# Kernel optimization log

Measured on AMD Instinct MI355X. Metric: run time of the kernel, lower is better.

## Reference

```python
import jax, jax.numpy as jnp
import numpy as np

K = 7       # kernel_size (window is K x K, padding=(K-1)//2, stride=1)
HEADS = 4   # number of heads; mid_channels = C // HEADS


def _unfold(x, k):
    # Emulates nn.Unfold(k, padding=(k-1)//2, stride=1) followed by reshape to
    # (B, C, P, H, W) with P = k*k ordered as (ki, kj) per channel (torch order).
    B, C, H, W = x.shape
    p = (k - 1) // 2
    xp = jnp.pad(x, ((0, 0), (0, 0), (p, p), (p, p)))  # zeros padding_mode
    patches = [xp[:, :, i:i + H, j:j + W] for i in range(k) for j in range(k)]
    return jnp.stack(patches, axis=2)  # (B, C, P, H, W)


def setup_inputs() -> dict:
    key = jax.random.key(0)
    x = jax.random.normal(key, (4, 64, 128, 128), dtype=jnp.float32)
    return {"x": x}


def reference(x):
    B, C, H, W = x.shape
    mid = C // HEADS
    P = K * K
    # (B, heads, mid, P, H, W)
    x_unf = _unfold(x, K).reshape(B, HEADS, mid, P, H, W)
    x_r = x.reshape(B, HEADS, mid, H, W)
    # squared L2 distance between center pixel feature and each window patch pixel
    A = ((x_unf ** 2).sum(axis=2)
         + (x_r ** 2).sum(axis=2, keepdims=True)
         - 2.0 * jnp.einsum('bgcphw,bgchw->bgphw', x_unf, x_r))  # (B,G,P,H,W)
    A = jax.nn.softmax(-A, axis=2)
    y = jnp.einsum('bgphw,bgcphw->bgchw', A, x_unf).reshape(B, C, H, W)
    return x + y  # residual=True
```

## Files before the change

### kernel.cpp

```cpp
#include <hip/hip_runtime.h>


#define TILE 16
#define RAD  3
#define HALO (TILE + 2 * RAD)
#define MID  16
#define NPIX (HALO * HALO)
#define IMG  128
#define HW   (IMG * IMG)
#define PSTR 20

__global__ __launch_bounds__(256, 4)
void nlm_kernel(const float* __restrict__ x, float* __restrict__ out) {
    const int g   = blockIdx.z & 3;
    const int b   = blockIdx.z >> 2;
    const int tx0 = blockIdx.x * TILE;
    const int ty0 = blockIdx.y * TILE;

    __shared__ __align__(16) float lds[NPIX * PSTR];

    const int tid = threadIdx.x;
    const float* xb = x + (size_t)(b * 64 + g * MID) * HW;

    for (int i = tid; i < NPIX * MID; i += 256) {
        const int c   = i / NPIX;
        const int pix = i - c * NPIX;
        const int yy  = pix / HALO;
        const int xx  = pix - yy * HALO;
        const int gy  = ty0 + yy - RAD;
        const int gx  = tx0 + xx - RAD;
        float v = 0.0f;
        if ((unsigned)gy < (unsigned)IMG && (unsigned)gx < (unsigned)IMG)
            v = xb[c * HW + gy * IMG + gx];
        lds[pix * PSTR + c] = v;
    }
    __syncthreads();

    for (int pix = tid; pix < NPIX; pix += 256) {
        const float* p = &lds[pix * PSTR];
        float ss = 0.0f;
        #pragma unroll
        for (int k = 0; k < 4; ++k) {
            const float4 v = *reinterpret_cast<const float4*>(p + 4 * k);
            ss = fmaf(v.x, v.x, ss); ss = fmaf(v.y, v.y, ss);
            ss = fmaf(v.z, v.z, ss); ss = fmaf(v.w, v.w, ss);
        }
        lds[pix * PSTR + MID] = ss;
    }
    __syncthreads();

    const int lx = tid & 15;
    const int ly = tid >> 4;
    const float* base = &lds[(ly * HALO + lx) * PSTR];

    float ctr[MID];
    {
        const float* cp = base + (RAD * HALO + RAD) * PSTR;
        #pragma unroll
        for (int k = 0; k < 4; ++k) {
            const float4 v = *reinterpret_cast<const float4*>(cp + 4 * k);
            ctr[4 * k + 0] = v.x; ctr[4 * k + 1] = v.y;
            ctr[4 * k + 2] = v.z; ctr[4 * k + 3] = v.w;
        }
    }
    const float cc = base[(RAD * HALO + RAD) * PSTR + MID];

    float acc[MID];
    #pragma unroll
    for (int c = 0; c < MID; ++c) acc[c] = 0.0f;
    float s = 0.0f;

    #pragma unroll
    for (int dy = 0; dy < 7; ++dy) {
        #pragma unroll
        for (int dx = 0; dx < 7; ++dx) {
            const float* nbp = base + (dy * HALO + dx) * PSTR;
            float nb[MID];
            #pragma unroll
            for (int k = 0; k < 4; ++k) {
                const float4 v = *reinterpret_cast<const float4*>(nbp + 4 * k);
                nb[4 * k + 0] = v.x; nb[4 * k + 1] = v.y;
                nb[4 * k + 2] = v.z; nb[4 * k + 3] = v.w;
            }
            const float nn = nbp[MID];
            float dot = 0.0f;
            #pragma unroll
            for (int c = 0; c < MID; ++c) dot = fmaf(nb[c], ctr[c], dot);
            const float w = __expf(fmaf(2.0f, dot, -(nn + cc)));
            s += w;
            #pragma unroll
            for (int c = 0; c < MID; ++c) acc[c] = fmaf(w, nb[c], acc[c]);
        }
    }

    const float inv = 1.0f / s;
    float* ob = out + (size_t)(b * 64 + g * MID) * HW
                    + (size_t)(ty0 + ly) * IMG + (tx0 + lx);
    #pragma unroll
    for (int c = 0; c < MID; ++c)
        ob[c * HW] = fmaf(acc[c], inv, ctr[c]);
}

extern "C" void kernel_launch(void* const* d_in, const int* in_sizes, int n_in,
                              void* d_out, int out_size, void* d_ws, size_t ws_size,
                              hipStream_t stream) {
    const float* x = (const float*)d_in[0];
    float* out = (float*)d_out;
    dim3 grid(IMG / TILE, IMG / TILE, 16);
    nlm_kernel<<<grid, 256, 0, stream>>>(x, out);
}
```

Before: 34.67 us.

## Compute two vertically adjacent pixels per thread to share neighbor LDS loads

Each thread now computes two vertically stacked output pixels, so each neighbor row loaded from LDS serves both pixels across the 8 overlapping window rows. The tile grows to 16x32 with a 22x38 halo, the halo fill loads 4 channels per thread and writes them as a float4, and squared norms move to a separate LDS array. This cuts LDS reads per pixel, at the cost of doubled accumulator registers, lower occupancy (launch bounds 2), half as many blocks, and more LDS per block.

New measurement: 29.58 us. 14.7% less time.

```diff
diff --git a/kernel.cpp b/kernel.cpp
--- a/kernel.cpp
+++ b/kernel.cpp
@@ -1,104 +1,145 @@
 #include <hip/hip_runtime.h>
 
 
-#define TILE 16
+#define TW   16
+#define TH   32
 #define RAD  3
-#define HALO (TILE + 2 * RAD)
+#define HWD  22
+#define HHT  38
 #define MID  16
-#define NPIX (HALO * HALO)
+#define NPIX (HWD * HHT)
+#define PSTR 20
 #define IMG  128
-#define HW   (IMG * IMG)
-#define PSTR 20
+#define PLANE (IMG * IMG)
 
-__global__ __launch_bounds__(256, 4)
+#define VISIT(RP, NP, WX, DO0, DO1)                                         \
+    {                                                                       \
+        const float* _rp = (RP) + (WX) * PSTR;                              \
+        float nb[MID];                                                      \
+        _Pragma("unroll")                                                   \
+        for (int k = 0; k < 4; ++k) {                                       \
+            const float4 v = *reinterpret_cast<const float4*>(_rp + 4 * k); \
+            nb[4*k+0] = v.x; nb[4*k+1] = v.y;                               \
+            nb[4*k+2] = v.z; nb[4*k+3] = v.w;                               \
+        }                                                                   \
+        const float nv = (NP)[WX];                                          \
+        if (DO0) {                                                          \
+            float dot = 0.f;                                                \
+            _Pragma("unroll")                                               \
+            for (int c = 0; c < MID; ++c) dot = fmaf(nb[c], ctr0[c], dot);  \
+            const float w = __expf(fmaf(2.f, dot, -(nv + cc0)));            \
+            s0 += w;                                                        \
+            _Pragma("unroll")                                               \
+            for (int c = 0; c < MID; ++c) acc0[c] = fmaf(w, nb[c], acc0[c]);\
+        }                                                                   \
+        if (DO1) {                                                          \
+            float dot = 0.f;                                                \
+            _Pragma("unroll")                                               \
+            for (int c = 0; c < MID; ++c) dot = fmaf(nb[c], ctr1[c], dot);  \
+            const float w = __expf(fmaf(2.f, dot, -(nv + cc1)));            \
+            s1 += w;                                                        \
+            _Pragma("unroll")                                               \
+            for (int c = 0; c < MID; ++c) acc1[c] = fmaf(w, nb[c], acc1[c]);\
+        }                                                                   \
+    }
+
+__global__ __launch_bounds__(256, 2)
 void nlm_kernel(const float* __restrict__ x, float* __restrict__ out) {
     const int g   = blockIdx.z & 3;
     const int b   = blockIdx.z >> 2;
-    const int tx0 = blockIdx.x * TILE;
-    const int ty0 = blockIdx.y * TILE;
+    const int tx0 = blockIdx.x * TW;
+    const int ty0 = blockIdx.y * TH;
 
-    __shared__ __align__(16) float lds[NPIX * PSTR];
+    __shared__ __align__(16) float rec[NPIX * PSTR];
+    __shared__ float nn[NPIX];
 
     const int tid = threadIdx.x;
-    const float* xb = x + (size_t)(b * 64 + g * MID) * HW;
+    const float* xb = x + (size_t)(b * 64 + g * MID) * PLANE;
 
-    for (int i = tid; i < NPIX * MID; i += 256) {
-        const int c   = i / NPIX;
-        const int pix = i - c * NPIX;
-        const int yy  = pix / HALO;
-        const int xx  = pix - yy * HALO;
+    for (int i = tid; i < 4 * NPIX; i += 256) {
+        const int cq  = i / NPIX;
+        const int pix = i - cq * NPIX;
+        const int yy  = pix / HWD;
+        const int xx  = pix - yy * HWD;
         const int gy  = ty0 + yy - RAD;
         const int gx  = tx0 + xx - RAD;
-        float v = 0.0f;
-        if ((unsigned)gy < (unsigned)IMG && (unsigned)gx < (unsigned)IMG)
-            v = xb[c * HW + gy * IMG + gx];
-        lds[pix * PSTR + c] = v;
+        float4 v = make_float4(0.f, 0.f, 0.f, 0.f);
+        if ((unsigned)gy < (unsigned)IMG && (unsigned)gx < (unsigned)IMG) {
+            const float* p = xb + (size_t)(4 * cq) * PLANE + gy * IMG + gx;
+            v.x = p[0];         v.y = p[PLANE];
+            v.z = p[2 * PLANE]; v.w = p[3 * PLANE];
+        }
+        *reinterpret_cast<float4*>(&rec[pix * PSTR + 4 * cq]) = v;
     }
     __syncthreads();
 
     for (int pix = tid; pix < NPIX; pix += 256) {
-        const float* p = &lds[pix * PSTR];
-        float ss = 0.0f;
+        const float* p = &rec[pix * PSTR];
+        float ss = 0.f;
         #pragma unroll
         for (int k = 0; k < 4; ++k) {
             const float4 v = *reinterpret_cast<const float4*>(p + 4 * k);
             ss = fmaf(v.x, v.x, ss); ss = fmaf(v.y, v.y, ss);
             ss = fmaf(v.z, v.z, ss); ss = fmaf(v.w, v.w, ss);
         }
-        lds[pix * PSTR + MID] = ss;
+        nn[pix] = ss;
     }
     __syncthreads();
 
-    const int lx = tid & 15;
-    const int ly = tid >> 4;
-    const float* base = &lds[(ly * HALO + lx) * PSTR];
+    const int lx  = tid & 15;
+    const int ly  = tid >> 4;
+    const int p00 = (2 * ly) * HWD + lx;
 
-    float ctr[MID];
+    float ctr0[MID], ctr1[MID];
     {
-        const float* cp = base + (RAD * HALO + RAD) * PSTR;
+        const float* c0 = &rec[(p00 + 3 * HWD + 3) * PSTR];
         #pragma unroll
         for (int k = 0; k < 4; ++k) {
-            const float4 v = *reinterpret_cast<const float4*>(cp + 4 * k);
-            ctr[4 * k + 0] = v.x; ctr[4 * k + 1] = v.y;
-            ctr[4 * k + 2] = v.z; ctr[4 * k + 3] = v.w;
+            const float4 v0 = *reinterpret_cast<const float4*>(c0 + 4 * k);
+            const float4 v1 = *reinterpret_cast<const float4*>(c0 + HWD * PSTR + 4 * k);
+            ctr0[4*k+0] = v0.x; ctr0[4*k+1] = v0.y;
+            ctr0[4*k+2] = v0.z; ctr0[4*k+3] = v0.w;
+            ctr1[4*k+0] = v1.x; ctr1[4*k+1] = v1.y;
+            ctr1[4*k+2] = v1.z; ctr1[4*k+3] = v1.w;
         }
     }
-    const float cc = base[(RAD * HALO + RAD) * PSTR + MID];
+    const float cc0 = nn[p00 + 3 * HWD + 3];
+    const float cc1 = nn[p00 + 4 * HWD + 3];
 
-    float acc[MID];
+    float acc0[MID], acc1[MID];
     #pragma unroll
-    for (int c = 0; c < MID; ++c) acc[c] = 0.0f;
-    float s = 0.0f;
+    for (int c = 0; c < MID; ++c) { acc0[c] = 0.f; acc1[c] = 0.f; }
+    float s0 = 0.f, s1 = 0.f;
 
-    #pragma unroll
-    for (int dy = 0; dy < 7; ++dy) {
+    {
+        const float* rp = &rec[p00 * PSTR];
+        const float* np = &nn[p00];
         #pragma unroll
-        for (int dx = 0; dx < 7; ++dx) {
-            const float* nbp = base + (dy * HALO + dx) * PSTR;
-            float nb[MID];
-            #pragma unroll
-            for (int k = 0; k < 4; ++k) {
-                const float4 v = *reinterpret_cast<const float4*>(nbp + 4 * k);
-                nb[4 * k + 0] = v.x; nb[4 * k + 1] = v.y;
-                nb[4 * k + 2] = v.z; nb[4 * k + 3] = v.w;
-            }
-            const float nn = nbp[MID];
-            float dot = 0.0f;
-            #pragma unroll
-            for (int c = 0; c < MID; ++c) dot = fmaf(nb[c], ctr[c], dot);
-            const float w = __expf(fmaf(2.0f, dot, -(nn + cc)));
-            s += w;
-            #pragma unroll
-            for (int c = 0; c < MID; ++c) acc[c] = fmaf(w, nb[c], acc[c]);
-        }
+        for (int wx = 0; wx < 7; ++wx) VISIT(rp, np, wx, true, false);
+    }
+    #pragma unroll 2
+    for (int wy = 1; wy < 7; ++wy) {
+        const float* rp = &rec[(p00 + wy * HWD) * PSTR];
+        const float* np = &nn[p00 + wy * HWD];
+        #pragma unroll
+        for (int wx = 0; wx < 7; ++wx) VISIT(rp, np, wx, true, true);
+    }
+    {
+        const float* rp = &rec[(p00 + 7 * HWD) * PSTR];
+        const float* np = &nn[p00 + 7 * HWD];
+        #pragma unroll
+        for (int wx = 0; wx < 7; ++wx) VISIT(rp, np, wx, false, true);
     }
 
-    const float inv = 1.0f / s;
-    float* ob = out + (size_t)(b * 64 + g * MID) * HW
-                    + (size_t)(ty0 + ly) * IMG + (tx0 + lx);
+    const float i0 = 1.f / s0;
+    const float i1 = 1.f / s1;
+    float* ob = out + (size_t)(b * 64 + g * MID) * PLANE
+                    + (size_t)(ty0 + 2 * ly) * IMG + (tx0 + lx);
     #pragma unroll
-    for (int c = 0; c < MID; ++c)
-        ob[c * HW] = fmaf(acc[c], inv, ctr[c]);
+    for (int c = 0; c < MID; ++c) {
+        ob[c * PLANE]       = fmaf(acc0[c], i0, ctr0[c]);
+        ob[c * PLANE + IMG] = fmaf(acc1[c], i1, ctr1[c]);
+    }
 }
 
 extern "C" void kernel_launch(void* const* d_in, const int* in_sizes, int n_in,
@@ -106,6 +147,6 @@
                               hipStream_t stream) {
     const float* x = (const float*)d_in[0];
     float* out = (float*)d_out;
-    dim3 grid(IMG / TILE, IMG / TILE, 16);
+    dim3 grid(IMG / TW, IMG / TH, 16);
     nlm_kernel<<<grid, 256, 0, stream>>>(x, out);
 }
```

## Store halo tile in LDS as packed bf16 and fuse load with norm computation

Applied to the files above, without the earlier changes.

The shared-memory halo tile now holds neighbour features as round-to-nearest bf16 pairs packed into 32-bit words, with the squared norms kept in a separate fp32 array. This halves LDS footprint and the read traffic in the 49-tap inner loop. The separate norm pass and its barrier are folded into the global load loop, and center features are read straight from global memory in full fp32. The dot product and weight sum are split into independent accumulators to shorten dependency chains, while the inner loop pays extra unpack shifts and masks and loses accuracy to bf16 rounding of the neighbour features.

Result: slower. 106.3 us (+206.6%).

```diff
diff --git a/kernel.cpp b/kernel.cpp
--- a/kernel.cpp
+++ b/kernel.cpp
@@ -1,104 +1,128 @@
 #include <hip/hip_runtime.h>
 
 
-#define TILE 16
-#define RAD  3
-#define HALO (TILE + 2 * RAD)
-#define MID  16
-#define NPIX (HALO * HALO)
-#define IMG  128
-#define HW   (IMG * IMG)
-#define PSTR 20
+#define TW    16
+#define RAD   3
+#define HWD   22
+#define NPIX  (HWD * HWD)
+#define MID   16
+#define PSTRD 10
+#define IMG   128
+#define PLANE (IMG * IMG)
+
+__device__ __forceinline__ unsigned bf16rne(float v) {
+    unsigned u = __float_as_uint(v);
+    u += 0x7fffu + ((u >> 16) & 1u);
+    return u >> 16;
+}
 
 __global__ __launch_bounds__(256, 4)
 void nlm_kernel(const float* __restrict__ x, float* __restrict__ out) {
     const int g   = blockIdx.z & 3;
     const int b   = blockIdx.z >> 2;
-    const int tx0 = blockIdx.x * TILE;
-    const int ty0 = blockIdx.y * TILE;
+    const int tx0 = blockIdx.x * TW;
+    const int ty0 = blockIdx.y * TW;
 
-    __shared__ __align__(16) float lds[NPIX * PSTR];
+    __shared__ __align__(16) unsigned recd[NPIX * PSTRD];
+    __shared__ float nn[NPIX];
 
     const int tid = threadIdx.x;
-    const float* xb = x + (size_t)(b * 64 + g * MID) * HW;
+    const int lx  = tid & 15;
+    const int ly  = tid >> 4;
+    const float* xb = x + (size_t)(b * 64 + g * MID) * PLANE;
 
-    for (int i = tid; i < NPIX * MID; i += 256) {
-        const int c   = i / NPIX;
-        const int pix = i - c * NPIX;
-        const int yy  = pix / HALO;
-        const int xx  = pix - yy * HALO;
-        const int gy  = ty0 + yy - RAD;
-        const int gx  = tx0 + xx - RAD;
-        float v = 0.0f;
-        if ((unsigned)gy < (unsigned)IMG && (unsigned)gx < (unsigned)IMG)
-            v = xb[c * HW + gy * IMG + gx];
-        lds[pix * PSTR + c] = v;
+    const float* cp = xb + (ty0 + ly) * IMG + (tx0 + lx);
+    float ctr[MID];
+    #pragma unroll
+    for (int c = 0; c < MID; ++c) ctr[c] = cp[c * PLANE];
+    float ccA = 0.f, ccB = 0.f;
+    #pragma unroll
+    for (int c = 0; c < MID; c += 2) {
+        ccA = fmaf(ctr[c], ctr[c], ccA);
+        ccB = fmaf(ctr[c + 1], ctr[c + 1], ccB);
+    }
+    const float cc = ccA + ccB;
+
+    for (int i = tid; i < NPIX; i += 256) {
+        const int yy = i / HWD;
+        const int xx = i - yy * HWD;
+        const int gy = ty0 + yy - RAD;
+        const int gx = tx0 + xx - RAD;
+        const bool in = ((unsigned)gy < (unsigned)IMG) & ((unsigned)gx < (unsigned)IMG);
+        const float* p = xb + gy * IMG + gx;
+        unsigned pk[8];
+        float ss = 0.f;
+        #pragma unroll
+        for (int k = 0; k < 8; ++k) {
+            const float v0 = in ? p[(2 * k) * PLANE] : 0.f;
+            const float v1 = in ? p[(2 * k + 1) * PLANE] : 0.f;
+            const unsigned q0 = bf16rne(v0);
+            const unsigned q1 = bf16rne(v1);
+            pk[k] = q0 | (q1 << 16);
+            const float r0 = __uint_as_float(q0 << 16);
+            const float r1 = __uint_as_float(q1 << 16);
+            ss = fmaf(r0, r0, ss);
+            ss = fmaf(r1, r1, ss);
+        }
+        unsigned* rp = &recd[i * PSTRD];
+        #pragma unroll
+        for (int k = 0; k < 4; ++k)
+            *reinterpret_cast<uint2*>(rp + 2 * k) = make_uint2(pk[2 * k], pk[2 * k + 1]);
+        nn[i] = ss;
     }
     __syncthreads();
 
-    for (int pix = tid; pix < NPIX; pix += 256) {
-        const float* p = &lds[pix * PSTR];
-        float ss = 0.0f;
-        #pragma unroll
-        for (int k = 0; k < 4; ++k) {
-            const float4 v = *reinterpret_cast<const float4*>(p + 4 * k);
-            ss = fmaf(v.x, v.x, ss); ss = fmaf(v.y, v.y, ss);
-            ss = fmaf(v.z, v.z, ss); ss = fmaf(v.w, v.w, ss);
-        }
-        lds[pix * PSTR + MID] = ss;
-    }
-    __syncthreads();
-
-    const int lx = tid & 15;
-    const int ly = tid >> 4;
-    const float* base = &lds[(ly * HALO + lx) * PSTR];
-
-    float ctr[MID];
-    {
-        const float* cp = base + (RAD * HALO + RAD) * PSTR;
-        #pragma unroll
-        for (int k = 0; k < 4; ++k) {
-            const float4 v = *reinterpret_cast<const float4*>(cp + 4 * k);
-            ctr[4 * k + 0] = v.x; ctr[4 * k + 1] = v.y;
-            ctr[4 * k + 2] = v.z; ctr[4 * k + 3] = v.w;
-        }
-    }
-    const float cc = base[(RAD * HALO + RAD) * PSTR + MID];
-
     float acc[MID];
     #pragma unroll
-    for (int c = 0; c < MID; ++c) acc[c] = 0.0f;
-    float s = 0.0f;
+    for (int c = 0; c < MID; ++c) acc[c] = 0.f;
+    float sA = 0.f, sB = 0.f;
 
-    #pragma unroll
-    for (int dy = 0; dy < 7; ++dy) {
+    for (int wy = 0; wy < 7; ++wy) {
+        const unsigned* rowp = &recd[((ly + wy) * HWD + lx) * PSTRD];
+        const float*    nrow = &nn[(ly + wy) * HWD + lx];
         #pragma unroll
-        for (int dx = 0; dx < 7; ++dx) {
-            const float* nbp = base + (dy * HALO + dx) * PSTR;
+        for (int wx = 0; wx < 7; ++wx) {
+            const unsigned* rp = rowp + wx * PSTRD;
+            const uint2 p0 = *reinterpret_cast<const uint2*>(rp + 0);
+            const uint2 p1 = *reinterpret_cast<const uint2*>(rp + 2);
+            const uint2 p2 = *reinterpret_cast<const uint2*>(rp + 4);
+            const uint2 p3 = *reinterpret_cast<const uint2*>(rp + 6);
             float nb[MID];
+            {
+                const unsigned w0 = p0.x, w1 = p0.y, w2 = p1.x, w3 = p1.y;
+                const unsigned w4 = p2.x, w5 = p2.y, w6 = p3.x, w7 = p3.y;
+                nb[0]  = __uint_as_float(w0 << 16); nb[1]  = __uint_as_float(w0 & 0xffff0000u);
+                nb[2]  = __uint_as_float(w1 << 16); nb[3]  = __uint_as_float(w1 & 0xffff0000u);
+                nb[4]  = __uint_as_float(w2 << 16); nb[5]  = __uint_as_float(w2 & 0xffff0000u);
+                nb[6]  = __uint_as_float(w3 << 16); nb[7]  = __uint_as_float(w3 & 0xffff0000u);
+                nb[8]  = __uint_as_float(w4 << 16); nb[9]  = __uint_as_float(w4 & 0xffff0000u);
+                nb[10] = __uint_as_float(w5 << 16); nb[11] = __uint_as_float(w5 & 0xffff0000u);
+                nb[12] = __uint_as_float(w6 << 16); nb[13] = __uint_as_float(w6 & 0xffff0000u);
+                nb[14] = __uint_as_float(w7 << 16); nb[15] = __uint_as_float(w7 & 0xffff0000u);
+            }
+            float d0 = 0.f, d1 = 0.f, d2 = 0.f, d3 = 0.f;
             #pragma unroll
-            for (int k = 0; k < 4; ++k) {
-                const float4 v = *reinterpret_cast<const float4*>(nbp + 4 * k);
-                nb[4 * k + 0] = v.x; nb[4 * k + 1] = v.y;
-                nb[4 * k + 2] = v.z; nb[4 * k + 3] = v.w;
+            for (int c = 0; c < MID; c += 4) {
+                d0 = fmaf(nb[c + 0], ctr[c + 0], d0);
+                d1 = fmaf(nb[c + 1], ctr[c + 1], d1);
+                d2 = fmaf(nb[c + 2], ctr[c + 2], d2);
+                d3 = fmaf(nb[c + 3], ctr[c + 3], d3);
             }
-            const float nn = nbp[MID];
-            float dot = 0.0f;
-            #pragma unroll
-            for (int c = 0; c < MID; ++c) dot = fmaf(nb[c], ctr[c], dot);
-            const float w = __expf(fmaf(2.0f, dot, -(nn + cc)));
-            s += w;
+            const float dot = (d0 + d1) + (d2 + d3);
+            const float a = fmaf(2.f, dot, -(nrow[wx] + cc));
+            const float w = __expf(a);
+            if (wx & 1) sB += w; else sA += w;
             #pragma unroll
             for (int c = 0; c < MID; ++c) acc[c] = fmaf(w, nb[c], acc[c]);
         }
     }
 
-    const float inv = 1.0f / s;
-    float* ob = out + (size_t)(b * 64 + g * MID) * HW
+    const float inv = 1.f / (sA + sB);
+    float* ob = out + (size_t)(b * 64 + g * MID) * PLANE
                     + (size_t)(ty0 + ly) * IMG + (tx0 + lx);
     #pragma unroll
     for (int c = 0; c < MID; ++c)
-        ob[c * HW] = fmaf(acc[c], inv, ctr[c]);
+        ob[c * PLANE] = fmaf(acc[c], inv, ctr[c]);
 }
 
 extern "C" void kernel_launch(void* const* d_in, const int* in_sizes, int n_in,
@@ -106,6 +130,6 @@
                               hipStream_t stream) {
     const float* x = (const float*)d_in[0];
     float* out = (float*)d_out;
-    dim3 grid(IMG / TILE, IMG / TILE, 16);
+    dim3 grid(IMG / TW, IMG / TW, 16);
     nlm_kernel<<<grid, 256, 0, stream>>>(x, out);
 }
```
